# Kernel tuning notes

Measured on AMD Instinct MI355X. Metric: run time of the kernel, lower is better.

The kernel has to match this reference:

```python
import jax, jax.numpy as jnp
import numpy as np

B, D, H = 1024, 128, 512


def _made_masks(D, H):
    # Canonical MADE degrees with natural ordering.
    m_in = np.arange(1, D + 1)                       # input degrees 1..D
    m_hid = (np.arange(H) % (D - 1)) + 1             # hidden degrees in [1, D-1]
    m_out = np.concatenate([np.arange(1, D + 1)] * 2)  # output degrees, repeated for (sigma, mu)
    M1 = (m_hid[:, None] >= m_in[None, :]).astype(np.float32)   # [H, D]
    M2 = (m_out[:, None] > m_hid[None, :]).astype(np.float32)   # [2D, H]
    return jnp.asarray(M1), jnp.asarray(M2)


def setup_inputs() -> dict:
    key = jax.random.key(0)
    k1, k2, k3 = jax.random.split(key, 3)
    x = jax.random.normal(k1, (B, D), dtype=jnp.float32)
    # small init so exp(sigma) stays numerically tame
    W1 = jax.random.normal(k2, (H, D), dtype=jnp.float32) * 0.05
    b1 = jnp.zeros((H,), dtype=jnp.float32)
    W2 = jax.random.normal(k3, (2 * D, H), dtype=jnp.float32) * 0.05
    b2 = jnp.zeros((2 * D,), dtype=jnp.float32)
    return {"x": x, "W1": W1, "b1": b1, "W2": W2, "b2": b2}


def reference(x, W1, b1, W2, b2):
    Din = x.shape[1]
    Hid = W1.shape[0]
    M1, M2 = _made_masks(Din, Hid)

    def made(z):
        h = jax.nn.relu(z @ (W1 * M1).T + b1)   # [B, H]
        return h @ (W2 * M2).T + b2              # [B, 2D]

    # backward_flow: sequential inversion, one dim per step (kl_forward=True)
    def step(carry, d):
        z, log_det = carry
        res = made(z)
        sigma = res[:, :Din]
        mu = res[:, Din:]
        s_d = jnp.take(sigma, d, axis=1)
        m_d = jnp.take(mu, d, axis=1)
        x_d = jnp.take(x, d, axis=1)
        z = z.at[:, d].set((x_d - m_d) * jnp.exp(-s_d))
        return (z, log_det - s_d), None

    init = (jnp.zeros_like(x), jnp.zeros((x.shape[0],), dtype=x.dtype))
    (z, log_det), _ = jax.lax.scan(step, init, jnp.arange(Din))
    return z, log_det
```

## Files before the change

kernel.cpp:

```cpp
#include <hip/hip_runtime.h>
#include <stdint.h>


#define Bz  1024
#define Dd  128
#define Hh  512
#define LN2 0.6931471805599453f
#define NRL -1.4426950408889634f

typedef float v4f __attribute__((ext_vector_type(4)));
typedef float v2f __attribute__((ext_vector_type(2)));

#define LOQ(q) __builtin_shufflevector(q, q, 0, 1)
#define HIQ(q) __builtin_shufflevector(q, q, 2, 3)

template<int CTRL, int RMASK>
__device__ __forceinline__ float dpp_add(float v) {
    int t = __builtin_amdgcn_update_dpp(0, __float_as_int(v), CTRL, RMASK, 0xf, true);
    return v + __int_as_float(t);
}
__device__ __forceinline__ float wave_sum63(float v) {
    v = dpp_add<0x111, 0xf>(v);
    v = dpp_add<0x112, 0xf>(v);
    v = dpp_add<0x114, 0xf>(v);
    v = dpp_add<0x118, 0xf>(v);
    v = dpp_add<0x142, 0xa>(v);
    v = dpp_add<0x143, 0xc>(v);
    return v;
}
__device__ __forceinline__ float bcast_lane(float v, int l) {
    return __int_as_float(__builtin_amdgcn_readlane(__float_as_int(v), l));
}
__device__ __forceinline__ float wave_sum_bcast(float v) {
    return bcast_lane(wave_sum63(v), 63);
}

__global__ void pack_kernel(const float* __restrict__ W1,
                            const float* __restrict__ W2,
                            const float* __restrict__ b2,
                            float* __restrict__ Wp) {
    int idx = blockIdx.x * blockDim.x + threadIdx.x;
    if (idx >= Dd * Hh) return;
    int d = idx >> 9, h = idx & 511;
    int mh = (h % 127) + 1;
    float* bp = Wp + d * 1536;
    bp[h]        = W2[d * Hh + h] * ((mh <= d) ? NRL : 0.f);
    bp[512 + h]  = W2[(Dd + d) * Hh + h] * ((mh <= d) ? 1.f : 0.f);
    bp[1024 + h] = W1[h * Dd + d] * ((mh > d) ? __expf(-b2[d]) : 0.f);
}

struct WBuf { v4f s0, s1, m0, m1, w0, w1; };

__device__ __forceinline__ void loadbuf(WBuf &b, const float* p) {
    b.s0 = *(const v4f*)(p);
    b.s1 = *(const v4f*)(p + 4);
    b.m0 = *(const v4f*)(p + 512);
    b.m1 = *(const v4f*)(p + 516);
    b.w0 = *(const v4f*)(p + 1024);
    b.w1 = *(const v4f*)(p + 1028);
    __builtin_amdgcn_sched_barrier(0);
}

__device__ __forceinline__ void stepD(int u, int lane,
    v2f (&a2)[4], const WBuf &w, float xa, float xb,
    float &za, float &zb, float &ldet63)
{
    const v2f zz = {0.f, 0.f};
    v2f h0 = __builtin_elementwise_max(a2[0], zz);
    v2f h1 = __builtin_elementwise_max(a2[1], zz);
    v2f h2 = __builtin_elementwise_max(a2[2], zz);
    v2f h3 = __builtin_elementwise_max(a2[3], zz);

    v2f psA = zz, psB = zz, pmA = zz, pmB = zz;
    psA = __builtin_elementwise_fma(h0, (v2f)LOQ(w.s0), psA);
    pmA = __builtin_elementwise_fma(h0, (v2f)LOQ(w.m0), pmA);
    psB = __builtin_elementwise_fma(h1, (v2f)HIQ(w.s0), psB);
    pmB = __builtin_elementwise_fma(h1, (v2f)HIQ(w.m0), pmB);
    psA = __builtin_elementwise_fma(h2, (v2f)LOQ(w.s1), psA);
    pmA = __builtin_elementwise_fma(h2, (v2f)LOQ(w.m1), pmA);
    psB = __builtin_elementwise_fma(h3, (v2f)HIQ(w.s1), psB);
    pmB = __builtin_elementwise_fma(h3, (v2f)HIQ(w.m1), pmB);
    v2f psp = psA + psB;
    v2f pmp = pmA + pmB;

    float sp = wave_sum63(psp.x + psp.y);
    float sm = wave_sum63(pmp.x + pmp.y);

    int dl = u & 63;
    float xv = bcast_lane(u < 64 ? xa : xb, dl);
    float zd63 = (xv - sm) * __builtin_amdgcn_exp2f(sp);
    ldet63 += sp;
    float zd = bcast_lane(zd63, 63);
    if (dl == lane) { if (u < 64) za = zd; else zb = zd; }

    v2f zd2 = {zd, zd};
    a2[0] = __builtin_elementwise_fma(zd2, (v2f)LOQ(w.w0), a2[0]);
    a2[1] = __builtin_elementwise_fma(zd2, (v2f)HIQ(w.w0), a2[1]);
    a2[2] = __builtin_elementwise_fma(zd2, (v2f)LOQ(w.w1), a2[2]);
    a2[3] = __builtin_elementwise_fma(zd2, (v2f)HIQ(w.w1), a2[3]);
}

__global__ __launch_bounds__(64, 1) void iaf13_kernel(
    const float* __restrict__ x,
    const float* __restrict__ b1,
    const float* __restrict__ b2,
    const float* __restrict__ Wp,
    float* __restrict__ out)
{
    const int lane = (int)threadIdx.x;
    const int row  = (int)blockIdx.x;
    const int h0   = lane * 8;

    v2f a2[4];
    {
        v4f t0v = *(const v4f*)(b1 + h0);
        v4f t1v = *(const v4f*)(b1 + h0 + 4);
        a2[0] = LOQ(t0v); a2[1] = HIQ(t0v);
        a2[2] = LOQ(t1v); a2[3] = HIQ(t1v);
    }
    float bsa = b2[lane],       bsb = b2[64 + lane];
    float bma = b2[128 + lane], bmb = b2[192 + lane];
    float xa  = x[row * Dd + lane]      - bma;
    float xb  = x[row * Dd + 64 + lane] - bmb;
    float Ea  = __builtin_amdgcn_exp2f(bsa * NRL);
    float Eb  = __builtin_amdgcn_exp2f(bsb * NRL);
    float Csum = NRL * wave_sum_bcast(bsa + bsb);

    float za = 0.f, zb = 0.f, ldet = 0.f;

    const float* base = Wp + h0;
    WBuf A, B, C;
    loadbuf(A, base + 0 * 1536);
    loadbuf(B, base + 1 * 1536);
    loadbuf(C, base + 2 * 1536);

#pragma unroll 1
    for (int t = 0; t < Dd - 2; t += 3) {
        stepD(t + 0, lane, a2, A, xa, xb, za, zb, ldet);
        loadbuf(A, base + (size_t)(t + 3) * 1536);
        stepD(t + 1, lane, a2, B, xa, xb, za, zb, ldet);
        loadbuf(B, base + (size_t)(t + 4) * 1536);
        stepD(t + 2, lane, a2, C, xa, xb, za, zb, ldet);
        loadbuf(C, base + (size_t)((t + 5 < Dd) ? (t + 5) : 0) * 1536);
    }
    stepD(Dd - 2, lane, a2, A, xa, xb, za, zb, ldet);
    stepD(Dd - 1, lane, a2, B, xa, xb, za, zb, ldet);

    out[row * Dd + lane]      = za * Ea;
    out[row * Dd + 64 + lane] = zb * Eb;
    float ldt = bcast_lane(ldet, 63);
    if (lane == 0) out[Bz * Dd + row] = LN2 * (ldt + Csum);
}

__global__ __launch_bounds__(64, 1) void iaf_fb_kernel(
    const float* __restrict__ x,  const float* __restrict__ W1,
    const float* __restrict__ b1, const float* __restrict__ W2,
    const float* __restrict__ b2, float* __restrict__ out)
{
    const int lane = (int)threadIdx.x;
    const int row  = (int)blockIdx.x;
    const int h0   = lane * 8;
    float a[8]; int mh[8];
#pragma unroll
    for (int k = 0; k < 8; ++k) { a[k] = b1[h0 + k]; mh[k] = ((h0 + k) % 127) + 1; }
    float xa  = x[row * Dd + lane], xb = x[row * Dd + 64 + lane];
    float b2a = b2[lane], b2b = b2[64 + lane], b2c = b2[128 + lane], b2d_ = b2[192 + lane];
    float za = 0.f, zb = 0.f, ld = 0.f;
    for (int d = 0; d < Dd; ++d) {
        float ps = 0.f, pm = 0.f;
#pragma unroll
        for (int k = 0; k < 8; ++k) {
            float h = fmaxf(a[k], 0.f);
            h = (mh[k] <= d) ? h : 0.f;
            ps = fmaf(h, W2[d * Hh + h0 + k], ps);
            pm = fmaf(h, W2[(Dd + d) * Hh + h0 + k], pm);
        }
        ps = wave_sum_bcast(ps);
        pm = wave_sum_bcast(pm);
        int dl = d & 63;
        float sd = ps + bcast_lane(d < 64 ? b2a : b2b, dl);
        float md = pm + bcast_lane(d < 64 ? b2c : b2d_, dl);
        float xv =      bcast_lane(d < 64 ? xa  : xb,  dl);
        float zd = (xv - md) * __expf(-sd);
        ld -= sd;
        if (dl == lane) { if (d < 64) za = zd; else zb = zd; }
#pragma unroll
        for (int k = 0; k < 8; ++k)
            if (d < mh[k]) a[k] = fmaf(zd, W1[(h0 + k) * Dd + d], a[k]);
    }
    out[row * Dd + lane]      = za;
    out[row * Dd + 64 + lane] = zb;
    if (lane == 0) out[Bz * Dd + row] = ld;
}

extern "C" void kernel_launch(void* const* d_in, const int* in_sizes, int n_in,
                              void* d_out, int out_size, void* d_ws, size_t ws_size,
                              hipStream_t stream) {
    const float* x  = (const float*)d_in[0];
    const float* W1 = (const float*)d_in[1];
    const float* b1 = (const float*)d_in[2];
    const float* W2 = (const float*)d_in[3];
    const float* b2 = (const float*)d_in[4];
    float* out = (float*)d_out;
    float* Wp  = (float*)d_ws;

    const size_t need = (size_t)Dd * 1536 * sizeof(float);
    if (ws_size >= need) {
        pack_kernel<<<(Dd * Hh + 255) / 256, 256, 0, stream>>>(W1, W2, b2, Wp);
        iaf13_kernel<<<Bz, 64, 0, stream>>>(x, b1, b2, Wp, out);
    } else {
        iaf_fb_kernel<<<Bz, 64, 0, stream>>>(x, W1, b1, W2, b2, out);
    }
}
```

Before: 33.03 us.

## Deepen weight prefetch to eight steps and fold x into mu reduction

Raises the register prefetch depth of packed per-step weights from three to eight buffers, so global loads have more steps of latency to hide behind. It also negates the mu weights and adds x into the selected lane's partial sum before the wave reduction, which removes a readlane and a subtract from the serial critical path. The loop is split into two halves so the lane index and the x/z register choice are fixed per half, removing the per-step selects. Register use rises from about 72 to about 192 VGPRs, which matters little at one wave per block but grows the code size.

Result: slower. 33.72 us (+2.1%).

```diff
diff --git a/kernel.cpp b/kernel.cpp
--- a/kernel.cpp
+++ b/kernel.cpp
@@ -45,7 +45,7 @@
     int mh = (h % 127) + 1;
     float* bp = Wp + d * 1536;
     bp[h]        = W2[d * Hh + h] * ((mh <= d) ? NRL : 0.f);
-    bp[512 + h]  = W2[(Dd + d) * Hh + h] * ((mh <= d) ? 1.f : 0.f);
+    bp[512 + h]  = -W2[(Dd + d) * Hh + h] * ((mh <= d) ? 1.f : 0.f);
     bp[1024 + h] = W1[h * Dd + d] * ((mh > d) ? __expf(-b2[d]) : 0.f);
 }
 
@@ -61,9 +61,9 @@
     __builtin_amdgcn_sched_barrier(0);
 }
 
-__device__ __forceinline__ void stepD(int u, int lane,
-    v2f (&a2)[4], const WBuf &w, float xa, float xb,
-    float &za, float &zb, float &ldet63)
+__device__ __forceinline__ void stepD(int dl, int lane,
+    v2f (&a2)[4], const WBuf &w, float xv,
+    float &zcap, float &ldet63)
 {
     const v2f zz = {0.f, 0.f};
     v2f h0 = __builtin_elementwise_max(a2[0], zz);
@@ -83,15 +83,19 @@
     v2f psp = psA + psB;
     v2f pmp = pmA + pmB;
 
-    float sp = wave_sum63(psp.x + psp.y);
-    float sm = wave_sum63(pmp.x + pmp.y);
-
-    int dl = u & 63;
-    float xv = bcast_lane(u < 64 ? xa : xb, dl);
-    float zd63 = (xv - sm) * __builtin_amdgcn_exp2f(sp);
+    float pspart = psp.x + psp.y;
+    float pmpart = pmp.x + pmp.y;
+
+    bool sel = (lane == dl);
+    pmpart += sel ? xv : 0.f;
+
+    float sp = wave_sum63(pspart);
+    float sm = wave_sum63(pmpart);
+
+    float zd63 = sm * __builtin_amdgcn_exp2f(sp);
     ldet63 += sp;
     float zd = bcast_lane(zd63, 63);
-    if (dl == lane) { if (u < 64) za = zd; else zb = zd; }
+    if (sel) zcap = zd;
 
     v2f zd2 = {zd, zd};
     a2[0] = __builtin_elementwise_fma(zd2, (v2f)LOQ(w.w0), a2[0]);
@@ -100,7 +104,7 @@
     a2[3] = __builtin_elementwise_fma(zd2, (v2f)HIQ(w.w1), a2[3]);
 }
 
-__global__ __launch_bounds__(64, 1) void iaf13_kernel(
+__global__ __launch_bounds__(64, 1) void iaf14_kernel(
     const float* __restrict__ x,
     const float* __restrict__ b1,
     const float* __restrict__ b2,
@@ -129,22 +133,46 @@
     float za = 0.f, zb = 0.f, ldet = 0.f;
 
     const float* base = Wp + h0;
-    WBuf A, B, C;
-    loadbuf(A, base + 0 * 1536);
-    loadbuf(B, base + 1 * 1536);
-    loadbuf(C, base + 2 * 1536);
+    WBuf W0, W1r, W2r, W3, W4, W5, W6, W7;
+    loadbuf(W0,  base + 0 * 1536);
+    loadbuf(W1r, base + 1 * 1536);
+    loadbuf(W2r, base + 2 * 1536);
+    loadbuf(W3,  base + 3 * 1536);
+    loadbuf(W4,  base + 4 * 1536);
+    loadbuf(W5,  base + 5 * 1536);
+    loadbuf(W6,  base + 6 * 1536);
+    loadbuf(W7,  base + 7 * 1536);
 
 #pragma unroll 1
-    for (int t = 0; t < Dd - 2; t += 3) {
-        stepD(t + 0, lane, a2, A, xa, xb, za, zb, ldet);
-        loadbuf(A, base + (size_t)(t + 3) * 1536);
-        stepD(t + 1, lane, a2, B, xa, xb, za, zb, ldet);
-        loadbuf(B, base + (size_t)(t + 4) * 1536);
-        stepD(t + 2, lane, a2, C, xa, xb, za, zb, ldet);
-        loadbuf(C, base + (size_t)((t + 5 < Dd) ? (t + 5) : 0) * 1536);
-    }
-    stepD(Dd - 2, lane, a2, A, xa, xb, za, zb, ldet);
-    stepD(Dd - 1, lane, a2, B, xa, xb, za, zb, ldet);
+    for (int t = 0; t < 64; t += 8) {
+        stepD(t + 0, lane, a2, W0,  xa, za, ldet); loadbuf(W0,  base + (size_t)(t +  8) * 1536);
+        stepD(t + 1, lane, a2, W1r, xa, za, ldet); loadbuf(W1r, base + (size_t)(t +  9) * 1536);
+        stepD(t + 2, lane, a2, W2r, xa, za, ldet); loadbuf(W2r, base + (size_t)(t + 10) * 1536);
+        stepD(t + 3, lane, a2, W3,  xa, za, ldet); loadbuf(W3,  base + (size_t)(t + 11) * 1536);
+        stepD(t + 4, lane, a2, W4,  xa, za, ldet); loadbuf(W4,  base + (size_t)(t + 12) * 1536);
+        stepD(t + 5, lane, a2, W5,  xa, za, ldet); loadbuf(W5,  base + (size_t)(t + 13) * 1536);
+        stepD(t + 6, lane, a2, W6,  xa, za, ldet); loadbuf(W6,  base + (size_t)(t + 14) * 1536);
+        stepD(t + 7, lane, a2, W7,  xa, za, ldet); loadbuf(W7,  base + (size_t)(t + 15) * 1536);
+    }
+#pragma unroll 1
+    for (int t = 0; t < 56; t += 8) {
+        stepD(t + 0, lane, a2, W0,  xb, zb, ldet); loadbuf(W0,  base + (size_t)(t + 72) * 1536);
+        stepD(t + 1, lane, a2, W1r, xb, zb, ldet); loadbuf(W1r, base + (size_t)(t + 73) * 1536);
+        stepD(t + 2, lane, a2, W2r, xb, zb, ldet); loadbuf(W2r, base + (size_t)(t + 74) * 1536);
+        stepD(t + 3, lane, a2, W3,  xb, zb, ldet); loadbuf(W3,  base + (size_t)(t + 75) * 1536);
+        stepD(t + 4, lane, a2, W4,  xb, zb, ldet); loadbuf(W4,  base + (size_t)(t + 76) * 1536);
+        stepD(t + 5, lane, a2, W5,  xb, zb, ldet); loadbuf(W5,  base + (size_t)(t + 77) * 1536);
+        stepD(t + 6, lane, a2, W6,  xb, zb, ldet); loadbuf(W6,  base + (size_t)(t + 78) * 1536);
+        stepD(t + 7, lane, a2, W7,  xb, zb, ldet); loadbuf(W7,  base + (size_t)(t + 79) * 1536);
+    }
+    stepD(56, lane, a2, W0,  xb, zb, ldet);
+    stepD(57, lane, a2, W1r, xb, zb, ldet);
+    stepD(58, lane, a2, W2r, xb, zb, ldet);
+    stepD(59, lane, a2, W3,  xb, zb, ldet);
+    stepD(60, lane, a2, W4,  xb, zb, ldet);
+    stepD(61, lane, a2, W5,  xb, zb, ldet);
+    stepD(62, lane, a2, W6,  xb, zb, ldet);
+    stepD(63, lane, a2, W7,  xb, zb, ldet);
 
     out[row * Dd + lane]      = za * Ea;
     out[row * Dd + 64 + lane] = zb * Eb;
@@ -207,7 +235,7 @@
     const size_t need = (size_t)Dd * 1536 * sizeof(float);
     if (ws_size >= need) {
         pack_kernel<<<(Dd * Hh + 255) / 256, 256, 0, stream>>>(W1, W2, b2, Wp);
-        iaf13_kernel<<<Bz, 64, 0, stream>>>(x, b1, b2, Wp, out);
+        iaf14_kernel<<<Bz, 64, 0, stream>>>(x, b1, b2, Wp, out);
     } else {
         iaf_fb_kernel<<<Bz, 64, 0, stream>>>(x, W1, b1, W2, b2, out);
     }
```

## Pack MADE weights as bf16 pairs and deepen prefetch ring to eight steps

Applied to the files above, without the earlier changes.

The pack kernel now stores the masked, pre-scaled weights as rounded bf16 pairs in 32-bit words, which halves the per-step weight footprint. The main kernel unpacks them with shifts and masks before the FMAs. The register prefetch ring grows from three to eight step buffers, which hides more load latency in the sequential 128-step loop. The cost is reduced weight precision, which can drift across 128 dependent steps, plus extra ALU work for unpacking and higher register pressure.

Result: slower. 35.13 us (+6.4%).

```diff
diff --git a/kernel.cpp b/kernel.cpp
--- a/kernel.cpp
+++ b/kernel.cpp
@@ -10,6 +10,7 @@
 
 typedef float v4f __attribute__((ext_vector_type(4)));
 typedef float v2f __attribute__((ext_vector_type(2)));
+typedef uint32_t v4u __attribute__((ext_vector_type(4)));
 
 #define LOQ(q) __builtin_shufflevector(q, q, 0, 1)
 #define HIQ(q) __builtin_shufflevector(q, q, 2, 3)
@@ -35,29 +36,45 @@
     return bcast_lane(wave_sum63(v), 63);
 }
 
+__device__ __forceinline__ uint32_t f2bf(float f) {
+    uint32_t u = __float_as_uint(f);
+    return (u + 0x7fffu + ((u >> 16) & 1u)) >> 16;
+}
+__device__ __forceinline__ v2f unpk(uint32_t u) {
+    v2f r;
+    r.x = __uint_as_float(u << 16);
+    r.y = __uint_as_float(u & 0xffff0000u);
+    return r;
+}
+
 __global__ void pack_kernel(const float* __restrict__ W1,
                             const float* __restrict__ W2,
                             const float* __restrict__ b2,
-                            float* __restrict__ Wp) {
+                            uint32_t* __restrict__ Wp) {
     int idx = blockIdx.x * blockDim.x + threadIdx.x;
-    if (idx >= Dd * Hh) return;
-    int d = idx >> 9, h = idx & 511;
-    int mh = (h % 127) + 1;
-    float* bp = Wp + d * 1536;
-    bp[h]        = W2[d * Hh + h] * ((mh <= d) ? NRL : 0.f);
-    bp[512 + h]  = W2[(Dd + d) * Hh + h] * ((mh <= d) ? 1.f : 0.f);
-    bp[1024 + h] = W1[h * Dd + d] * ((mh > d) ? __expf(-b2[d]) : 0.f);
-}
-
-struct WBuf { v4f s0, s1, m0, m1, w0, w1; };
-
-__device__ __forceinline__ void loadbuf(WBuf &b, const float* p) {
-    b.s0 = *(const v4f*)(p);
-    b.s1 = *(const v4f*)(p + 4);
-    b.m0 = *(const v4f*)(p + 512);
-    b.m1 = *(const v4f*)(p + 516);
-    b.w0 = *(const v4f*)(p + 1024);
-    b.w1 = *(const v4f*)(p + 1028);
+    if (idx >= Dd * 768) return;
+    int d = idx / 768, w = idx % 768;
+    int seg = w >> 8, p = w & 255;
+    uint32_t lohi[2];
+#pragma unroll
+    for (int j = 0; j < 2; ++j) {
+        int h  = 2 * p + j;
+        int mh = (h % 127) + 1;
+        float v;
+        if (seg == 0)      v = W2[d * Hh + h]        * ((mh <= d) ? NRL : 0.f);
+        else if (seg == 1) v = W2[(Dd + d) * Hh + h] * ((mh <= d) ? 1.f : 0.f);
+        else               v = W1[h * Dd + d] * ((mh > d) ? __expf(-b2[d]) : 0.f);
+        lohi[j] = f2bf(v);
+    }
+    Wp[(size_t)d * 768 + w] = lohi[0] | (lohi[1] << 16);
+}
+
+struct WBuf { v4u s, m, w; };
+
+__device__ __forceinline__ void loadbuf(WBuf &b, const uint32_t* p) {
+    b.s = *(const v4u*)(p);
+    b.m = *(const v4u*)(p + 256);
+    b.w = *(const v4u*)(p + 512);
     __builtin_amdgcn_sched_barrier(0);
 }
 
@@ -72,14 +89,14 @@
     v2f h3 = __builtin_elementwise_max(a2[3], zz);
 
     v2f psA = zz, psB = zz, pmA = zz, pmB = zz;
-    psA = __builtin_elementwise_fma(h0, (v2f)LOQ(w.s0), psA);
-    pmA = __builtin_elementwise_fma(h0, (v2f)LOQ(w.m0), pmA);
-    psB = __builtin_elementwise_fma(h1, (v2f)HIQ(w.s0), psB);
-    pmB = __builtin_elementwise_fma(h1, (v2f)HIQ(w.m0), pmB);
-    psA = __builtin_elementwise_fma(h2, (v2f)LOQ(w.s1), psA);
-    pmA = __builtin_elementwise_fma(h2, (v2f)LOQ(w.m1), pmA);
-    psB = __builtin_elementwise_fma(h3, (v2f)HIQ(w.s1), psB);
-    pmB = __builtin_elementwise_fma(h3, (v2f)HIQ(w.m1), pmB);
+    psA = __builtin_elementwise_fma(h0, unpk(w.s[0]), psA);
+    pmA = __builtin_elementwise_fma(h0, unpk(w.m[0]), pmA);
+    psB = __builtin_elementwise_fma(h1, unpk(w.s[1]), psB);
+    pmB = __builtin_elementwise_fma(h1, unpk(w.m[1]), pmB);
+    psA = __builtin_elementwise_fma(h2, unpk(w.s[2]), psA);
+    pmA = __builtin_elementwise_fma(h2, unpk(w.m[2]), pmA);
+    psB = __builtin_elementwise_fma(h3, unpk(w.s[3]), psB);
+    pmB = __builtin_elementwise_fma(h3, unpk(w.m[3]), pmB);
     v2f psp = psA + psB;
     v2f pmp = pmA + pmB;
 
@@ -94,17 +111,17 @@
     if (dl == lane) { if (u < 64) za = zd; else zb = zd; }
 
     v2f zd2 = {zd, zd};
-    a2[0] = __builtin_elementwise_fma(zd2, (v2f)LOQ(w.w0), a2[0]);
-    a2[1] = __builtin_elementwise_fma(zd2, (v2f)HIQ(w.w0), a2[1]);
-    a2[2] = __builtin_elementwise_fma(zd2, (v2f)LOQ(w.w1), a2[2]);
-    a2[3] = __builtin_elementwise_fma(zd2, (v2f)HIQ(w.w1), a2[3]);
-}
-
-__global__ __launch_bounds__(64, 1) void iaf13_kernel(
+    a2[0] = __builtin_elementwise_fma(zd2, unpk(w.w[0]), a2[0]);
+    a2[1] = __builtin_elementwise_fma(zd2, unpk(w.w[1]), a2[1]);
+    a2[2] = __builtin_elementwise_fma(zd2, unpk(w.w[2]), a2[2]);
+    a2[3] = __builtin_elementwise_fma(zd2, unpk(w.w[3]), a2[3]);
+}
+
+__global__ __launch_bounds__(64, 1) void iaf15_kernel(
     const float* __restrict__ x,
     const float* __restrict__ b1,
     const float* __restrict__ b2,
-    const float* __restrict__ Wp,
+    const uint32_t* __restrict__ Wp,
     float* __restrict__ out)
 {
     const int lane = (int)threadIdx.x;
@@ -128,23 +145,36 @@
 
     float za = 0.f, zb = 0.f, ldet = 0.f;
 
-    const float* base = Wp + h0;
-    WBuf A, B, C;
-    loadbuf(A, base + 0 * 1536);
-    loadbuf(B, base + 1 * 1536);
-    loadbuf(C, base + 2 * 1536);
+    const uint32_t* base = Wp + lane * 4;
+    WBuf B0, B1, B2, B3, B4, B5, B6, B7;
+    loadbuf(B0, base + 0 * 768);
+    loadbuf(B1, base + 1 * 768);
+    loadbuf(B2, base + 2 * 768);
+    loadbuf(B3, base + 3 * 768);
+    loadbuf(B4, base + 4 * 768);
+    loadbuf(B5, base + 5 * 768);
+    loadbuf(B6, base + 6 * 768);
+    loadbuf(B7, base + 7 * 768);
 
 #pragma unroll 1
-    for (int t = 0; t < Dd - 2; t += 3) {
-        stepD(t + 0, lane, a2, A, xa, xb, za, zb, ldet);
-        loadbuf(A, base + (size_t)(t + 3) * 1536);
-        stepD(t + 1, lane, a2, B, xa, xb, za, zb, ldet);
-        loadbuf(B, base + (size_t)(t + 4) * 1536);
-        stepD(t + 2, lane, a2, C, xa, xb, za, zb, ldet);
-        loadbuf(C, base + (size_t)((t + 5 < Dd) ? (t + 5) : 0) * 1536);
-    }
-    stepD(Dd - 2, lane, a2, A, xa, xb, za, zb, ldet);
-    stepD(Dd - 1, lane, a2, B, xa, xb, za, zb, ldet);
+    for (int t = 0; t < Dd; t += 8) {
+        stepD(t + 0, lane, a2, B0, xa, xb, za, zb, ldet);
+        loadbuf(B0, base + (size_t)((t +  8 < Dd) ? (t +  8) : 0) * 768);
+        stepD(t + 1, lane, a2, B1, xa, xb, za, zb, ldet);
+        loadbuf(B1, base + (size_t)((t +  9 < Dd) ? (t +  9) : 1) * 768);
+        stepD(t + 2, lane, a2, B2, xa, xb, za, zb, ldet);
+        loadbuf(B2, base + (size_t)((t + 10 < Dd) ? (t + 10) : 2) * 768);
+        stepD(t + 3, lane, a2, B3, xa, xb, za, zb, ldet);
+        loadbuf(B3, base + (size_t)((t + 11 < Dd) ? (t + 11) : 3) * 768);
+        stepD(t + 4, lane, a2, B4, xa, xb, za, zb, ldet);
+        loadbuf(B4, base + (size_t)((t + 12 < Dd) ? (t + 12) : 4) * 768);
+        stepD(t + 5, lane, a2, B5, xa, xb, za, zb, ldet);
+        loadbuf(B5, base + (size_t)((t + 13 < Dd) ? (t + 13) : 5) * 768);
+        stepD(t + 6, lane, a2, B6, xa, xb, za, zb, ldet);
+        loadbuf(B6, base + (size_t)((t + 14 < Dd) ? (t + 14) : 6) * 768);
+        stepD(t + 7, lane, a2, B7, xa, xb, za, zb, ldet);
+        loadbuf(B7, base + (size_t)((t + 15 < Dd) ? (t + 15) : 7) * 768);
+    }
 
     out[row * Dd + lane]      = za * Ea;
     out[row * Dd + 64 + lane] = zb * Eb;
@@ -202,12 +232,12 @@
     const float* W2 = (const float*)d_in[3];
     const float* b2 = (const float*)d_in[4];
     float* out = (float*)d_out;
-    float* Wp  = (float*)d_ws;
-
-    const size_t need = (size_t)Dd * 1536 * sizeof(float);
+    uint32_t* Wp = (uint32_t*)d_ws;
+
+    const size_t need = (size_t)Dd * 768 * sizeof(uint32_t);
     if (ws_size >= need) {
-        pack_kernel<<<(Dd * Hh + 255) / 256, 256, 0, stream>>>(W1, W2, b2, Wp);
-        iaf13_kernel<<<Bz, 64, 0, stream>>>(x, b1, b2, Wp, out);
+        pack_kernel<<<(Dd * 768 + 255) / 256, 256, 0, stream>>>(W1, W2, b2, Wp);
+        iaf15_kernel<<<Bz, 64, 0, stream>>>(x, b1, b2, Wp, out);
     } else {
         iaf_fb_kernel<<<Bz, 64, 0, stream>>>(x, W1, b1, W2, b2, out);
     }
```
